# Optimization experiments

Measured on AMD Instinct MI355X. Metric: run time of the kernel, lower is better.

## Reference

```python
import jax, jax.numpy as jnp
import numpy as np

IMAGE_W = 640
IMAGE_H = 640
ALPHA = 0.25
GAMMA = 2.0
BETA = 1.0 / 9.0
EPS = 1e-4


def _make_anchors(image_w, image_h):
    # standard RetinaNet anchors: 3 ratios x 3 scales per location, 5 FPN levels
    strides = [8, 16, 32, 64, 128]
    base_sizes = [32, 64, 128, 256, 512]
    ratios = np.array([0.5, 1.0, 2.0])
    scales = np.array([2.0 ** 0, 2.0 ** (1.0 / 3.0), 2.0 ** (2.0 / 3.0)])
    all_boxes = []
    for s, b in zip(strides, base_sizes):
        fw, fh = image_w // s, image_h // s
        ws, hs = [], []
        for r in ratios:
            for sc in scales:
                area = (b * sc) ** 2
                w = np.sqrt(area / r)
                ws.append(w)
                hs.append(w * r)
        wh = np.stack([np.array(ws), np.array(hs)], axis=-1).reshape(1, -1, 2)
        cx = (np.arange(fw) + 0.5) * s
        cy = (np.arange(fh) + 0.5) * s
        cx, cy = np.meshgrid(cx, cy)
        ctr = np.stack([cx, cy], axis=-1).reshape(-1, 1, 2)
        boxes = np.concatenate([ctr - 0.5 * wh, ctr + 0.5 * wh], axis=-1).reshape(-1, 4)
        all_boxes.append(boxes)
    return np.concatenate(all_boxes, axis=0).astype(np.float32)  # [76725, 4]


def setup_inputs() -> dict:
    key = jax.random.key(0)
    k1, k2, k3, k4, k5 = jax.random.split(key, 5)
    B, C, M = 4, 80, 16
    anchors = jnp.asarray(_make_anchors(IMAGE_W, IMAGE_H))  # [N,4]
    N = anchors.shape[0]
    batch_anchors = jnp.broadcast_to(anchors[None], (B, N, 4))
    cls_heads = jax.random.uniform(k1, (B, N, C), minval=0.01, maxval=0.99, dtype=jnp.float32)
    reg_heads = jax.random.normal(k2, (B, N, 4), dtype=jnp.float32)
    xy = jax.random.uniform(k3, (B, M, 2), minval=0.0, maxval=480.0)
    wh = jax.random.uniform(k4, (B, M, 2), minval=32.0, maxval=160.0)
    boxes = jnp.concatenate([xy, jnp.minimum(xy + wh, 639.0)], axis=-1)
    labels = jax.random.randint(k5, (B, M), 0, C).astype(jnp.float32)
    valid = jnp.arange(M)[None, :] < 12  # last 4 gt slots are -1 padding
    annotations = jnp.where(valid[..., None],
                            jnp.concatenate([boxes, labels[..., None]], axis=-1),
                            -1.0)
    return {"cls_heads": cls_heads, "reg_heads": reg_heads,
            "batch_anchors": batch_anchors, "annotations": annotations}


def _assign_one_image(anchors, annots):
    # anchors [N,4], annots [M,5] (label<0 == padding)
    valid_gt = annots[:, 4] >= 0.0                                  # [M]
    boxes, cls = annots[:, :4], annots[:, 4]
    area_a = (anchors[:, 2] - anchors[:, 0]) * (anchors[:, 3] - anchors[:, 1])
    area_g = (boxes[:, 2] - boxes[:, 0]) * (boxes[:, 3] - boxes[:, 1])
    lt = jnp.maximum(anchors[:, None, :2], boxes[None, :, :2])      # [N,M,2]
    rb = jnp.minimum(anchors[:, None, 2:], boxes[None, :, 2:])
    wh = jnp.clip(rb - lt, 0.0)
    inter = wh[..., 0] * wh[..., 1]                                 # [N,M]
    iou = inter / (area_a[:, None] + area_g[None, :] - inter)
    iou = jnp.where(valid_gt[None, :], iou, -1.0)                   # ignore padded gts
    idx = jnp.argmax(iou, axis=1)                                   # [N]
    overlap = jnp.max(iou, axis=1)
    gt_box = boxes[idx]                                             # [N,4]
    gt_cls = cls[idx]
    # encode gt box as (tx,ty,tw,th) wrt anchor
    a_wh = anchors[:, 2:] - anchors[:, :2]
    a_ctr = anchors[:, :2] + 0.5 * a_wh
    g_wh = jnp.clip(gt_box[:, 2:] - gt_box[:, :2], 1.0)
    g_ctr = gt_box[:, :2] + 0.5 * g_wh
    targets = jnp.concatenate([(g_ctr - a_ctr) / a_wh, jnp.log(g_wh / a_wh)], axis=1)
    targets = targets / jnp.array([0.1, 0.1, 0.2, 0.2], dtype=targets.dtype)
    label = jnp.full_like(overlap, -1.0)
    label = jnp.where(overlap < 0.4, 0.0, label)
    label = jnp.where(overlap > 0.5, gt_cls + 1.0, label)
    label = jnp.where(jnp.any(valid_gt), label, -1.0)               # no gt -> all ignore
    return targets, label


def reference(cls_heads, reg_heads, batch_anchors, annotations):
    # mask (instead of filter) out-of-border anchors: equivalent to dropping them
    a = batch_anchors
    inside = (a[..., 0] > 0) & (a[..., 1] > 0) & (a[..., 2] < IMAGE_W) & (a[..., 3] < IMAGE_H)
    targets, labels = jax.vmap(_assign_one_image)(batch_anchors, annotations)  # [B,N,4],[B,N]
    labels = jnp.where(inside, labels, -1.0)

    cls_mask = labels >= 0.0          # anchors counted in focal loss
    pos_mask = labels > 0.0           # positive anchors
    pos = jnp.sum(pos_mask, axis=1).astype(cls_heads.dtype)  # [B]

    # focal (cls) loss
    p = jnp.clip(cls_heads, EPS, 1.0 - EPS)                   # [B,N,C]
    num_classes = cls_heads.shape[-1]
    gt_onehot = jax.nn.one_hot(labels.astype(jnp.int32), num_classes + 1,
                               dtype=cls_heads.dtype)[..., 1:]  # [B,N,C]
    is_pos = gt_onehot > 0.5
    alpha_f = jnp.where(is_pos, ALPHA, 1.0 - ALPHA)
    pt = jnp.where(is_pos, p, 1.0 - p)
    focal_w = alpha_f * (1.0 - pt) ** GAMMA
    bce = -gt_onehot * jnp.log(p) - (1.0 - gt_onehot) * jnp.log(1.0 - p)
    fl = focal_w * bce
    cls_per_img = jnp.sum(fl * cls_mask[..., None], axis=(1, 2)) / jnp.maximum(pos, 1.0)

    # smooth-L1 (reg) loss over positive anchors
    x = jnp.abs(reg_heads - targets)
    sl1 = jnp.where(x < BETA, 0.5 * x * x / BETA, x - 0.5 * BETA)
    reg_per_img = jnp.sum(sl1 * pos_mask[..., None], axis=(1, 2)) / jnp.maximum(4.0 * pos, 1.0)

    valid_img = pos > 0.0
    n_valid = jnp.maximum(jnp.sum(valid_img.astype(cls_heads.dtype)), 1.0)
    cls_loss = jnp.sum(jnp.where(valid_img, cls_per_img, 0.0)) / n_valid
    reg_loss = jnp.sum(jnp.where(valid_img, reg_per_img, 0.0)) / n_valid
    return (cls_loss, reg_loss)
```

## Files before the change

kernel.cpp:

```cpp
#include <hip/hip_runtime.h>
#include <cmath>


typedef float fvec4 __attribute__((ext_vector_type(4)));

__device__ __forceinline__ void async_ld16(const float* g, float* l) {
    __builtin_amdgcn_global_load_lds(
        (const __attribute__((address_space(1))) unsigned int*)g,
        (__attribute__((address_space(3))) unsigned int*)l,
        16, 0, 0);
}

__global__ __launch_bounds__(256) void retina_main(
    const float* __restrict__ cls_heads,
    const float* __restrict__ reg_heads,
    const float* __restrict__ anchors,
    const float* __restrict__ annots,
    float* __restrict__ ws,
    int N, int M, int B)
{
    const int b  = blockIdx.y;
    const int n0 = blockIdx.x << 7;
    const int t  = threadIdx.x;

    __shared__ float s_cls[128 * 80];
    __shared__ float s_lab[128];
    __shared__ float s_red[12];

    const int tile   = (N - n0 < 128) ? (N - n0) : 128;
    const int valid4 = tile * 20;
    const float* gbase = cls_heads + ((size_t)b * N + n0) * 80;
    #pragma unroll
    for (int k = 0; k < 10; ++k) {
        const int idx  = (k << 8) + t;
        const int gidx = (idx < valid4) ? idx : 0;
        async_ld16(gbase + 4 * gidx, &s_cls[4 * idx]);
    }

    float reg_acc = 0.0f;
    float pos_cnt = 0.0f;
    float label   = -1.0f;
    if (t < 128) {
        const int n = n0 + t;
        if (n < N) {
            const float4 a = *(const float4*)(anchors + (size_t)n * 4);
            const bool inside = (a.x > 0.0f) && (a.y > 0.0f) &&
                                (a.z < 640.0f) && (a.w < 640.0f);
            if (inside) {
                const float* ann = annots + (size_t)b * 5 * M;
                const float area_a = (a.z - a.x) * (a.w - a.y);
                float best = -3.0e38f;
                int   bi   = 0;
                bool  any  = false;
                for (int m = 0; m < M; ++m) {
                    const float gx1 = ann[m*5+0], gy1 = ann[m*5+1];
                    const float gx2 = ann[m*5+2], gy2 = ann[m*5+3];
                    const float gc  = ann[m*5+4];
                    float v = -1.0f;
                    if (gc >= 0.0f) {
                        any = true;
                        const float iw = fmaxf(fminf(a.z, gx2) - fmaxf(a.x, gx1), 0.0f);
                        const float ih = fmaxf(fminf(a.w, gy2) - fmaxf(a.y, gy1), 0.0f);
                        const float inter = iw * ih;
                        v = inter / (area_a + (gx2 - gx1) * (gy2 - gy1) - inter);
                    }
                    if (v > best) { best = v; bi = m; }
                }
                if (any) {
                    if (best < 0.4f)      label = 0.0f;
                    else if (best > 0.5f) label = ann[bi*5+4] + 1.0f;
                }
                if (label > 0.0f) {
                    pos_cnt = 1.0f;
                    const float aw = a.z - a.x, ah = a.w - a.y;
                    const float acx = a.x + 0.5f * aw, acy = a.y + 0.5f * ah;
                    const float gw = fmaxf(ann[bi*5+2] - ann[bi*5+0], 1.0f);
                    const float gh = fmaxf(ann[bi*5+3] - ann[bi*5+1], 1.0f);
                    const float gcx = ann[bi*5+0] + 0.5f * gw;
                    const float gcy = ann[bi*5+1] + 0.5f * gh;
                    const float tx = (gcx - acx) / aw * 10.0f;
                    const float ty = (gcy - acy) / ah * 10.0f;
                    const float tw = __logf(gw / aw) * 5.0f;
                    const float th = __logf(gh / ah) * 5.0f;
                    const float4 r = *(const float4*)(reg_heads + ((size_t)b * N + n) * 4);
                    const float dx[4] = { fabsf(r.x - tx), fabsf(r.y - ty),
                                          fabsf(r.z - tw), fabsf(r.w - th) };
                    #pragma unroll
                    for (int j = 0; j < 4; ++j) {
                        const float x = dx[j];
                        reg_acc += (x < (1.0f / 9.0f)) ? 4.5f * x * x
                                                       : x - (1.0f / 18.0f);
                    }
                }
            }
        }
        s_lab[t] = label;
    }

    __builtin_amdgcn_s_waitcnt(0);
    const int anyValid = __syncthreads_or(label >= 0.0f ? 1 : 0);

    float cls_acc = 0.0f;
    if (anyValid) {
        #pragma unroll
        for (int k = 0; k < 10; ++k) {
            const int e  = (k << 8) + t;
            const int a  = e / 20;
            const int c4 = e - a * 20;
            const float lab = s_lab[a];
            if (lab >= 0.0f) {
                const fvec4 v = *(const fvec4*)&s_cls[4 * e];
                const float pv[4] = { v.x, v.y, v.z, v.w };
                const float cb = (float)(c4 * 4 + 1);
                float local = 0.0f;
                #pragma unroll
                for (int j = 0; j < 4; ++j) {
                    const float p = fminf(fmaxf(pv[j], 1.0e-4f), 1.0f - 1.0e-4f);
                    const bool  is_pos = (lab == cb + (float)j);
                    const float pt     = is_pos ? p : 1.0f - p;
                    const float alpha  = is_pos ? 0.25f : 0.75f;
                    const float om     = 1.0f - pt;
                    local += alpha * om * om * (-__logf(pt));
                }
                cls_acc += local;
            }
        }
    }

    const int lane = t & 63, wid = t >> 6;
    #pragma unroll
    for (int off = 32; off > 0; off >>= 1) {
        cls_acc += __shfl_down(cls_acc, off, 64);
        reg_acc += __shfl_down(reg_acc, off, 64);
        pos_cnt += __shfl_down(pos_cnt, off, 64);
    }
    if (lane == 0) {
        s_red[wid]     = cls_acc;
        s_red[4 + wid] = reg_acc;
        s_red[8 + wid] = pos_cnt;
    }
    __syncthreads();
    if (t == 0) {
        const float c = s_red[0] + s_red[1] + s_red[2]  + s_red[3];
        const float r = s_red[4] + s_red[5] + s_red[6]  + s_red[7];
        const float p = s_red[8] + s_red[9] + s_red[10] + s_red[11];
        if (c != 0.0f) atomicAdd(&ws[b], c);
        if (r != 0.0f) atomicAdd(&ws[B + b], r);
        if (p != 0.0f) atomicAdd(&ws[2 * B + b], p);
    }
}

__global__ void retina_final(const float* __restrict__ ws,
                             float* __restrict__ out, int B)
{
    if (threadIdx.x == 0 && blockIdx.x == 0) {
        float cl = 0.0f, rl = 0.0f, nv = 0.0f;
        for (int b = 0; b < B; ++b) {
            const float pos = ws[2 * B + b];
            if (pos > 0.0f) {
                cl += ws[b]     / fmaxf(pos, 1.0f);
                rl += ws[B + b] / fmaxf(4.0f * pos, 1.0f);
                nv += 1.0f;
            }
        }
        const float n = fmaxf(nv, 1.0f);
        out[0] = cl / n;
        out[1] = rl / n;
    }
}

extern "C" void kernel_launch(void* const* d_in, const int* in_sizes, int n_in,
                              void* d_out, int out_size, void* d_ws, size_t ws_size,
                              hipStream_t stream) {
    const float* cls = (const float*)d_in[0];
    const float* reg = (const float*)d_in[1];
    const float* anc = (const float*)d_in[2];
    const float* ann = (const float*)d_in[3];

    const int B = 4;
    const int N = in_sizes[1] / (4 * B);
    const int M = in_sizes[3] / (5 * B);
    float* ws = (float*)d_ws;

    (void)hipMemsetAsync(d_ws, 0, 12 * sizeof(float), stream);

    dim3 grid((N + 127) / 128, B);
    retina_main<<<grid, 256, 0, stream>>>(cls, reg, anc, ann, ws, N, M, B);
    retina_final<<<1, 64, 0, stream>>>(ws, (float*)d_out, B);
}
```

Measured before the change: 175.7 us.

## Load class scores directly to registers and double anchors per block

Drops the async global-to-LDS staging of class scores and instead issues ten independent float4 register loads per thread in two batches. The loads happen only after the label pass and only when the tile has valid anchors. Each block now covers 256 anchors, so all threads do assignment and there are half as many blocks and atomics. The cls loss is masked by multiplication instead of branching, and the workspace indices are hardcoded for B=4. This removes the 40KB LDS footprint, which should raise occupancy. The trade-off is that the memory loads no longer overlap with the IoU assignment work.

```diff
diff --git a/kernel.cpp b/kernel.cpp
--- a/kernel.cpp
+++ b/kernel.cpp
@@ -3,13 +3,6 @@
 
 
 typedef float fvec4 __attribute__((ext_vector_type(4)));
-
-__device__ __forceinline__ void async_ld16(const float* g, float* l) {
-    __builtin_amdgcn_global_load_lds(
-        (const __attribute__((address_space(1))) unsigned int*)g,
-        (__attribute__((address_space(3))) unsigned int*)l,
-        16, 0, 0);
-}
 
 __global__ __launch_bounds__(256) void retina_main(
     const float* __restrict__ cls_heads,
@@ -20,97 +13,120 @@
     int N, int M, int B)
 {
     const int b  = blockIdx.y;
-    const int n0 = blockIdx.x << 7;
+    const int n0 = blockIdx.x << 8;
     const int t  = threadIdx.x;
 
-    __shared__ float s_cls[128 * 80];
-    __shared__ float s_lab[128];
+    __shared__ float s_lab[256];
     __shared__ float s_red[12];
-
-    const int tile   = (N - n0 < 128) ? (N - n0) : 128;
-    const int valid4 = tile * 20;
-    const float* gbase = cls_heads + ((size_t)b * N + n0) * 80;
-    #pragma unroll
-    for (int k = 0; k < 10; ++k) {
-        const int idx  = (k << 8) + t;
-        const int gidx = (idx < valid4) ? idx : 0;
-        async_ld16(gbase + 4 * gidx, &s_cls[4 * idx]);
-    }
 
     float reg_acc = 0.0f;
     float pos_cnt = 0.0f;
     float label   = -1.0f;
-    if (t < 128) {
-        const int n = n0 + t;
-        if (n < N) {
-            const float4 a = *(const float4*)(anchors + (size_t)n * 4);
-            const bool inside = (a.x > 0.0f) && (a.y > 0.0f) &&
-                                (a.z < 640.0f) && (a.w < 640.0f);
-            if (inside) {
-                const float* ann = annots + (size_t)b * 5 * M;
-                const float area_a = (a.z - a.x) * (a.w - a.y);
-                float best = -3.0e38f;
-                int   bi   = 0;
-                bool  any  = false;
-                for (int m = 0; m < M; ++m) {
-                    const float gx1 = ann[m*5+0], gy1 = ann[m*5+1];
-                    const float gx2 = ann[m*5+2], gy2 = ann[m*5+3];
-                    const float gc  = ann[m*5+4];
-                    float v = -1.0f;
-                    if (gc >= 0.0f) {
-                        any = true;
-                        const float iw = fmaxf(fminf(a.z, gx2) - fmaxf(a.x, gx1), 0.0f);
-                        const float ih = fmaxf(fminf(a.w, gy2) - fmaxf(a.y, gy1), 0.0f);
-                        const float inter = iw * ih;
-                        v = inter / (area_a + (gx2 - gx1) * (gy2 - gy1) - inter);
-                    }
-                    if (v > best) { best = v; bi = m; }
+    const int n = n0 + t;
+    if (n < N) {
+        const float4 a = *(const float4*)(anchors + (size_t)n * 4);
+        const bool inside = (a.x > 0.0f) && (a.y > 0.0f) &&
+                            (a.z < 640.0f) && (a.w < 640.0f);
+        if (inside) {
+            const float* ann = annots + (size_t)b * 5 * M;
+            const float area_a = (a.z - a.x) * (a.w - a.y);
+            float best = -3.0e38f;
+            int   bi   = 0;
+            bool  any  = false;
+            for (int m = 0; m < M; ++m) {
+                const float gx1 = ann[m*5+0], gy1 = ann[m*5+1];
+                const float gx2 = ann[m*5+2], gy2 = ann[m*5+3];
+                const float gc  = ann[m*5+4];
+                float v = -1.0f;
+                if (gc >= 0.0f) {
+                    any = true;
+                    const float iw = fmaxf(fminf(a.z, gx2) - fmaxf(a.x, gx1), 0.0f);
+                    const float ih = fmaxf(fminf(a.w, gy2) - fmaxf(a.y, gy1), 0.0f);
+                    const float inter = iw * ih;
+                    v = inter / (area_a + (gx2 - gx1) * (gy2 - gy1) - inter);
                 }
-                if (any) {
-                    if (best < 0.4f)      label = 0.0f;
-                    else if (best > 0.5f) label = ann[bi*5+4] + 1.0f;
+                if (v > best) { best = v; bi = m; }
+            }
+            if (any) {
+                if (best < 0.4f)      label = 0.0f;
+                else if (best > 0.5f) label = ann[bi*5+4] + 1.0f;
+            }
+            if (label > 0.0f) {
+                pos_cnt = 1.0f;
+                const float aw = a.z - a.x, ah = a.w - a.y;
+                const float acx = a.x + 0.5f * aw, acy = a.y + 0.5f * ah;
+                const float gw = fmaxf(ann[bi*5+2] - ann[bi*5+0], 1.0f);
+                const float gh = fmaxf(ann[bi*5+3] - ann[bi*5+1], 1.0f);
+                const float gcx = ann[bi*5+0] + 0.5f * gw;
+                const float gcy = ann[bi*5+1] + 0.5f * gh;
+                const float tx = (gcx - acx) / aw * 10.0f;
+                const float ty = (gcy - acy) / ah * 10.0f;
+                const float tw = __logf(gw / aw) * 5.0f;
+                const float th = __logf(gh / ah) * 5.0f;
+                const float4 r = *(const float4*)(reg_heads + ((size_t)b * N + n) * 4);
+                const float dx[4] = { fabsf(r.x - tx), fabsf(r.y - ty),
+                                      fabsf(r.z - tw), fabsf(r.w - th) };
+                #pragma unroll
+                for (int j = 0; j < 4; ++j) {
+                    const float x = dx[j];
+                    reg_acc += (x < (1.0f / 9.0f)) ? 4.5f * x * x
+                                                   : x - (1.0f / 18.0f);
                 }
-                if (label > 0.0f) {
-                    pos_cnt = 1.0f;
-                    const float aw = a.z - a.x, ah = a.w - a.y;
-                    const float acx = a.x + 0.5f * aw, acy = a.y + 0.5f * ah;
-                    const float gw = fmaxf(ann[bi*5+2] - ann[bi*5+0], 1.0f);
-                    const float gh = fmaxf(ann[bi*5+3] - ann[bi*5+1], 1.0f);
-                    const float gcx = ann[bi*5+0] + 0.5f * gw;
-                    const float gcy = ann[bi*5+1] + 0.5f * gh;
-                    const float tx = (gcx - acx) / aw * 10.0f;
-                    const float ty = (gcy - acy) / ah * 10.0f;
-                    const float tw = __logf(gw / aw) * 5.0f;
-                    const float th = __logf(gh / ah) * 5.0f;
-                    const float4 r = *(const float4*)(reg_heads + ((size_t)b * N + n) * 4);
-                    const float dx[4] = { fabsf(r.x - tx), fabsf(r.y - ty),
-                                          fabsf(r.z - tw), fabsf(r.w - th) };
-                    #pragma unroll
-                    for (int j = 0; j < 4; ++j) {
-                        const float x = dx[j];
-                        reg_acc += (x < (1.0f / 9.0f)) ? 4.5f * x * x
-                                                       : x - (1.0f / 18.0f);
-                    }
-                }
             }
         }
-        s_lab[t] = label;
-    }
-
-    __builtin_amdgcn_s_waitcnt(0);
+    }
+    s_lab[t] = label;
     const int anyValid = __syncthreads_or(label >= 0.0f ? 1 : 0);
 
     float cls_acc = 0.0f;
     if (anyValid) {
+        const int tile   = (N - n0 < 256) ? (N - n0) : 256;
+        const int valid4 = tile * 20;
+        const float* cls_base = cls_heads + ((size_t)b * N + n0) * 80;
+
         #pragma unroll
-        for (int k = 0; k < 10; ++k) {
-            const int e  = (k << 8) + t;
-            const int a  = e / 20;
-            const int c4 = e - a * 20;
-            const float lab = s_lab[a];
-            if (lab >= 0.0f) {
-                const fvec4 v = *(const fvec4*)&s_cls[4 * e];
-                const float pv[4] = { v.x, v.y, v.z, v.w };
+        for (int h = 0; h < 2; ++h) {
+            float lb0,lb1,lb2,lb3,lb4,lb5,lb6,lb7,lb8,lb9;
+            {
+                const int e0 = t + (h * 10 + 0) * 256;
+                lb0 = s_lab[(e0            ) / 20];
+                lb1 = s_lab[(e0 +  1 * 256 ) / 20];
+                lb2 = s_lab[(e0 +  2 * 256 ) / 20];
+                lb3 = s_lab[(e0 +  3 * 256 ) / 20];
+                lb4 = s_lab[(e0 +  4 * 256 ) / 20];
+                lb5 = s_lab[(e0 +  5 * 256 ) / 20];
+                lb6 = s_lab[(e0 +  6 * 256 ) / 20];
+                lb7 = s_lab[(e0 +  7 * 256 ) / 20];
+                lb8 = s_lab[(e0 +  8 * 256 ) / 20];
+                lb9 = s_lab[(e0 +  9 * 256 ) / 20];
+            }
+            const int e0 = t + (h * 10 + 0) * 256;
+            #define CLMP(E) (((E) < valid4) ? (E) : 0)
+            const int a0 = CLMP(e0), a1 = CLMP(e0 + 256), a2 = CLMP(e0 + 512),
+                      a3 = CLMP(e0 + 768), a4 = CLMP(e0 + 1024), a5 = CLMP(e0 + 1280),
+                      a6 = CLMP(e0 + 1536), a7 = CLMP(e0 + 1792), a8 = CLMP(e0 + 2048),
+                      a9 = CLMP(e0 + 2304);
+            #undef CLMP
+            const fvec4 v0 = *(const fvec4*)(cls_base + 4 * a0);
+            const fvec4 v1 = *(const fvec4*)(cls_base + 4 * a1);
+            const fvec4 v2 = *(const fvec4*)(cls_base + 4 * a2);
+            const fvec4 v3 = *(const fvec4*)(cls_base + 4 * a3);
+            const fvec4 v4 = *(const fvec4*)(cls_base + 4 * a4);
+            const fvec4 v5 = *(const fvec4*)(cls_base + 4 * a5);
+            const fvec4 v6 = *(const fvec4*)(cls_base + 4 * a6);
+            const fvec4 v7 = *(const fvec4*)(cls_base + 4 * a7);
+            const fvec4 v8 = *(const fvec4*)(cls_base + 4 * a8);
+            const fvec4 v9 = *(const fvec4*)(cls_base + 4 * a9);
+
+            const float lbs[10] = {lb0,lb1,lb2,lb3,lb4,lb5,lb6,lb7,lb8,lb9};
+            const fvec4 vs[10]  = {v0,v1,v2,v3,v4,v5,v6,v7,v8,v9};
+            #pragma unroll
+            for (int k = 0; k < 10; ++k) {
+                const int e   = e0 + k * 256;
+                const int c4  = e - (e / 20) * 20;
+                const float lab  = lbs[k];
+                const float mask = (lab >= 0.0f) ? 1.0f : 0.0f;
+                const float pv[4] = { vs[k].x, vs[k].y, vs[k].z, vs[k].w };
                 const float cb = (float)(c4 * 4 + 1);
                 float local = 0.0f;
                 #pragma unroll
@@ -122,7 +138,7 @@
                     const float om     = 1.0f - pt;
                     local += alpha * om * om * (-__logf(pt));
                 }
-                cls_acc += local;
+                cls_acc += mask * local;
             }
         }
     }
@@ -145,8 +161,8 @@
         const float r = s_red[4] + s_red[5] + s_red[6]  + s_red[7];
         const float p = s_red[8] + s_red[9] + s_red[10] + s_red[11];
         if (c != 0.0f) atomicAdd(&ws[b], c);
-        if (r != 0.0f) atomicAdd(&ws[B + b], r);
-        if (p != 0.0f) atomicAdd(&ws[2 * B + b], p);
+        if (r != 0.0f) atomicAdd(&ws[4 + b], r);
+        if (p != 0.0f) atomicAdd(&ws[8 + b], p);
     }
 }
 
@@ -156,10 +172,10 @@
     if (threadIdx.x == 0 && blockIdx.x == 0) {
         float cl = 0.0f, rl = 0.0f, nv = 0.0f;
         for (int b = 0; b < B; ++b) {
-            const float pos = ws[2 * B + b];
+            const float pos = ws[8 + b];
             if (pos > 0.0f) {
                 cl += ws[b]     / fmaxf(pos, 1.0f);
-                rl += ws[B + b] / fmaxf(4.0f * pos, 1.0f);
+                rl += ws[4 + b] / fmaxf(4.0f * pos, 1.0f);
                 nv += 1.0f;
             }
         }
@@ -184,7 +200,7 @@
 
     (void)hipMemsetAsync(d_ws, 0, 12 * sizeof(float), stream);
 
-    dim3 grid((N + 127) / 128, B);
+    dim3 grid((N + 255) / 256, B);
     retina_main<<<grid, 256, 0, stream>>>(cls, reg, anc, ann, ws, N, M, B);
     retina_final<<<1, 64, 0, stream>>>(ws, (float*)d_out, B);
 }
```

New measurement: 169.2 us. 3.7% less time.
